# Optimization experiments

Measured on AMD Instinct MI355X. Metric: run time of the kernel, lower is better.

Reference implementation:

```python
import jax, jax.numpy as jnp
import numpy as np

N_NODES = 100000
D = 64        # graph_embed_size == utterance_embed_size
B = 64        # batch size == number of groups per layer
K = 500000    # selected candidate nodes per layer
M = 200000    # mention nodes
ATT_H = 20    # attention_hidden_dim
CTX = 4 * D   # context_embed_size = 2*graph + 2*utter


def setup_inputs() -> dict:
    key = jax.random.key(0)
    ks = jax.random.split(key, 16)
    graph_embed = jax.random.normal(ks[0], (N_NODES, D), jnp.float32)
    utterance_embed = jax.random.normal(ks[1], (B, D), jnp.float32)
    mention_index = jax.random.randint(ks[2], (M,), 0, N_NODES)
    mention_batch_index = jnp.sort(jax.random.randint(ks[3], (M,), 0, B))
    sel_indices = jax.random.randint(ks[4], (2, K), 0, N_NODES + 1)
    sel_batch_indices = jnp.sort(jax.random.randint(ks[5], (2, K), 0, B), axis=-1)
    sel_group_indices = jnp.sort(jax.random.randint(ks[6], (2, K), 0, B), axis=-1)
    grp_batch_indices = jnp.tile(jnp.arange(B), (2, 1))  # group i belongs to batch i
    last_indices = jax.random.randint(ks[7], (2, B), 0, N_NODES + 1)
    intent_indices = jax.random.randint(ks[8], (2, B), 0, 3)
    score_masks = jnp.ones((2, K), jnp.float32)
    # learned parameters (torch nn.Linear default init: U(-1/sqrt(fan_in), 1/sqrt(fan_in)))
    s_w = 1.0 / np.sqrt(D)
    s_v = 1.0 / np.sqrt(ATT_H)
    s_c = 1.0 / np.sqrt(CTX)
    att_W = jax.random.uniform(ks[9], (ATT_H, D), jnp.float32, -s_w, s_w)
    att_V = jax.random.uniform(ks[10], (1, ATT_H), jnp.float32, -s_v, s_v)
    W1_w = jax.random.uniform(ks[11], (1, CTX), jnp.float32, -s_c, s_c)
    W1_b = jax.random.uniform(ks[12], (1,), jnp.float32, -s_c, s_c)
    W2_w = jax.random.uniform(ks[13], (1, CTX), jnp.float32, -s_c, s_c)
    W2_b = jax.random.uniform(ks[14], (1,), jnp.float32, -s_c, s_c)
    intent_emb = jax.random.normal(ks[15], (3, D), jnp.float32)
    return dict(graph_embed=graph_embed, utterance_embed=utterance_embed,
                mention_index=mention_index, mention_batch_index=mention_batch_index,
                sel_indices=sel_indices, sel_batch_indices=sel_batch_indices,
                sel_group_indices=sel_group_indices, grp_batch_indices=grp_batch_indices,
                last_indices=last_indices, intent_indices=intent_indices,
                score_masks=score_masks, att_W=att_W, att_V=att_V,
                W1_w=W1_w, W1_b=W1_b, W2_w=W2_w, W2_b=W2_b, intent_emb=intent_emb)


def _segment_attention(embed, batch_index, att_W, att_V):
    # Self_Attention with batch_index: segment softmax + weighted segment sum.
    beta = jnp.squeeze(jnp.tanh(embed @ att_W.T) @ att_V.T, -1)      # [M]
    exp_beta = jnp.exp(beta)                                          # faithful: raw exp
    seg_sum = jax.ops.segment_sum(exp_beta, batch_index, num_segments=B)  # [B]
    alpha = exp_beta / seg_sum[batch_index]                           # [M]
    return jax.ops.segment_sum(alpha[:, None] * embed, batch_index, num_segments=B)  # [B,D]


def _layer(W_w, W_b, utter, portrait, graph_e, sel, sel_b, sel_g, grp_b,
           last, intent, mask, intent_emb, last_weight):
    context = jnp.concatenate([utter, portrait], axis=-1)             # [B,2D]
    feats = graph_e[sel]                                              # [K,D]
    # grp_context = [tiled context | start-point embed | intent embed] -> [G,4D]
    grp_ctx = jnp.concatenate([context[grp_b], graph_e[last], intent_emb[intent]], axis=-1)
    weights = jax.nn.sigmoid(grp_ctx @ W_w.T + W_b)                   # [G,1]
    tu = utter[sel_b]                                                 # [K,D]
    tp = portrait[sel_b]                                              # [K,D]
    w = weights[sel_g]                                                # [K,1]
    scores = jnp.sum((tu * w + tp * (1.0 - w)) * feats, axis=-1)      # [K]
    if last_weight is None:
        return scores, weights
    lw = last_weight[sel_b]                                           # [K,1]
    last_scores = jnp.sum((tu * lw + tp * (1.0 - lw)) * feats, axis=-1)
    return last_scores + mask * scores, None


def reference(graph_embed, utterance_embed, mention_index, mention_batch_index,
              sel_indices, sel_batch_indices, sel_group_indices, grp_batch_indices,
              last_indices, intent_indices, score_masks,
              att_W, att_V, W1_w, W1_b, W2_w, W2_b, intent_emb):
    # user portrait via segment-softmax attention over mentioned nodes
    mention_embed = graph_embed[mention_index]                        # [M,D]
    portrait = _segment_attention(mention_embed, mention_batch_index, att_W, att_V)  # [B,D]
    # extended graph embedding with abstract (zero) row appended
    graph_e = jnp.concatenate([graph_embed, jnp.zeros((1, D), graph_embed.dtype)], axis=0)
    s0, w0 = _layer(W1_w, W1_b, utterance_embed, portrait, graph_e,
                    sel_indices[0], sel_batch_indices[0], sel_group_indices[0],
                    grp_batch_indices[0], last_indices[0], intent_indices[0],
                    score_masks[0], intent_emb, None)
    s1, _ = _layer(W2_w, W2_b, utterance_embed, portrait, graph_e,
                   sel_indices[1], sel_batch_indices[1], sel_group_indices[1],
                   grp_batch_indices[1], last_indices[1], intent_indices[1],
                   score_masks[1], intent_emb, w0)
    return jnp.stack([s0, s1], axis=0)                                # [2,K]
```

## Files before the change

kernel.cpp:

```cpp
#include <hip/hip_runtime.h>
#include <math.h>

#define N_NODES 100000
#define D_EMB   64
#define KSEL    500000
#define NMENT   200000
#define ATT_H   20
#define NPAD    100352

#define WS_EB    0
#define WS_NUM   100000
#define WS_DEN   104096
#define WS_PORT  104160
#define WS_W     108256
#define WS_T     108544
#define WS_TOTAL_BYTES ((size_t)(WS_T + 64 * NPAD) * 4)

#define NPB 391
#define NBLK_G 784

typedef __attribute__((ext_vector_type(8))) short bf16x8;
typedef __attribute__((ext_vector_type(4))) float f32x4;

__device__ __forceinline__ unsigned pack2bf(float a, float b) {
    unsigned ua = __float_as_uint(a), ub = __float_as_uint(b);
    ua = (ua + 0x7FFFu + ((ua >> 16) & 1u)) >> 16;
    ub = (ub + 0x7FFFu + ((ub >> 16) & 1u)) >> 16;
    return ua | (ub << 16);
}
__device__ __forceinline__ float uasf(unsigned u) { return __uint_as_float(u); }

__global__ __launch_bounds__(256) void kP(const float* __restrict__ ge,
                                          const float* __restrict__ attW,
                                          const float* __restrict__ attV,
                                          float* __restrict__ ws) {
    int tid = blockIdx.x * 256 + threadIdx.x;
    if (tid < 64 * 64 + 64) ws[WS_NUM + tid] = 0.f;
    if (tid >= N_NODES) return;

    const float4* g4 = (const float4*)(ge + (size_t)tid * D_EMB);
    float4 x[16];
#pragma unroll
    for (int i = 0; i < 16; ++i) x[i] = g4[i];

    float beta = 0.f;
#pragma unroll
    for (int j = 0; j < ATT_H; ++j) {
        float h = 0.f;
#pragma unroll
        for (int i = 0; i < 16; ++i) {
            float4 w = ((const float4*)(attW + j * D_EMB))[i];
            h += w.x * x[i].x + w.y * x[i].y + w.z * x[i].z + w.w * x[i].w;
        }
        beta += attV[j] * tanhf(h);
    }
    ws[WS_EB + tid] = expf(beta);
}

__global__ __launch_bounds__(256, 8) void kA2n(const float* __restrict__ ge,
                                               const int* __restrict__ mi,
                                               const int* __restrict__ mbi,
                                               float* __restrict__ ws) {
    __shared__ float lacc[64 * 64];
    __shared__ float lden[64];
    for (int i = threadIdx.x; i < 64 * 64; i += 256) lacc[i] = 0.f;
    if (threadIdx.x < 64) lden[threadIdx.x] = 0.f;
    __syncthreads();

    int lane = threadIdx.x & 63;
    int grp  = lane >> 4, lp = lane & 15;
    int wave = blockIdx.x * 4 + (threadIdx.x >> 6);
    int s = wave * 25;

    bool valid = lane < 25;
    int lastB  = mbi[s + 24];
    int nd     = valid ? mi[s + lane] : 0;
    int bb     = valid ? mbi[s + lane] : lastB;
    float ebv  = valid ? ws[WS_EB + nd] : 0.f;
    int code   = nd | (bb << 17);

    int cd[7]; float e7[7]; float4 rr[7];
#pragma unroll
    for (int i = 0; i < 7; ++i) {
        int u = 4 * i + grp;
        cd[i] = __shfl(code, u);
        e7[i] = __shfl(ebv, u);
    }
#pragma unroll
    for (int i = 0; i < 7; ++i)
        rr[i] = *(const float4*)(ge + (size_t)(cd[i] & 0x1FFFF) * 64 + lp * 4);

    int curb = (__shfl(code, 0) >> 17) & 63;
    float4 acc = make_float4(0.f, 0.f, 0.f, 0.f);
    float dacc = 0.f;
#pragma unroll
    for (int i = 0; i < 7; ++i) {
        int u = 4 * i + grp;
        int b = (cd[i] >> 17) & 63;
        if (u < 25 && b != curb) {
            atomicAdd(&lacc[curb * 64 + lp * 4 + 0], acc.x);
            atomicAdd(&lacc[curb * 64 + lp * 4 + 1], acc.y);
            atomicAdd(&lacc[curb * 64 + lp * 4 + 2], acc.z);
            atomicAdd(&lacc[curb * 64 + lp * 4 + 3], acc.w);
            if (lp == 0) atomicAdd(&lden[curb], dacc);
            acc = make_float4(0.f, 0.f, 0.f, 0.f); dacc = 0.f; curb = b;
        }
        float e = e7[i];
        acc.x = fmaf(e, rr[i].x, acc.x);
        acc.y = fmaf(e, rr[i].y, acc.y);
        acc.z = fmaf(e, rr[i].z, acc.z);
        acc.w = fmaf(e, rr[i].w, acc.w);
        dacc += e;
    }
    atomicAdd(&lacc[curb * 64 + lp * 4 + 0], acc.x);
    atomicAdd(&lacc[curb * 64 + lp * 4 + 1], acc.y);
    atomicAdd(&lacc[curb * 64 + lp * 4 + 2], acc.z);
    atomicAdd(&lacc[curb * 64 + lp * 4 + 3], acc.w);
    if (lp == 0) atomicAdd(&lden[curb], dacc);
    __syncthreads();

    int sB = blockIdx.x * 100;
    int b0 = mbi[sB];
    int b1 = mbi[sB + 99];
    int nb = b1 - b0 + 1;
    for (int idx = threadIdx.x; idx < nb * 64; idx += 256) {
        int b2 = b0 + (idx >> 6), d = idx & 63;
        float v = lacc[b2 * 64 + d];
        if (v != 0.f) atomicAdd(&ws[WS_NUM + b2 * 64 + d], v);
    }
    if (threadIdx.x < nb) {
        float v = lden[b0 + threadIdx.x];
        if (v != 0.f) atomicAdd(&ws[WS_DEN + b0 + threadIdx.x], v);
    }
}

__global__ __launch_bounds__(64) void kBW(const float* __restrict__ ge,
                                          const float* __restrict__ utter,
                                          const int* __restrict__ grpb,
                                          const int* __restrict__ lastI,
                                          const int* __restrict__ intentI,
                                          const float* __restrict__ W1w,
                                          const float* __restrict__ W1b,
                                          const float* __restrict__ W2w,
                                          const float* __restrict__ W2b,
                                          const float* __restrict__ intentEmb,
                                          float* __restrict__ ws) {
    int bi = blockIdx.x;
    int l  = bi >> 6;
    int g  = bi & 63;
    int d  = threadIdx.x;

    if (l == 0) {
        ws[WS_PORT + g * 64 + d] = ws[WS_NUM + g * 64 + d] / ws[WS_DEN + g];
    }
    int gb = grpb[bi];
    float pd = ws[WS_NUM + gb * 64 + d] / ws[WS_DEN + gb];

    int last = lastI[bi];
    float gl = (last < N_NODES) ? ge[(size_t)last * D_EMB + d] : 0.f;
    int it = intentI[bi];
    float ie = intentEmb[it * D_EMB + d];

    const float* Ww = (l == 0) ? W1w : W2w;
    float bias      = (l == 0) ? W1b[0] : W2b[0];

    float val = utter[gb * D_EMB + d] * Ww[d]
              + pd * Ww[64 + d]
              + gl * Ww[128 + d]
              + ie * Ww[192 + d];
#pragma unroll
    for (int off = 32; off; off >>= 1) val += __shfl_xor(val, off);
    if (d == 0) ws[WS_W + bi] = 1.f / (1.f + expf(-(val + bias)));
}

__global__ __launch_bounds__(256) void kG(const float* __restrict__ ge,
                                          const float* __restrict__ utter,
                                          float* __restrict__ ws) {
    int nblk = blockIdx.x;

    __shared__ unsigned sQ[128 * 36];
    int tid = threadIdx.x;
    for (int i = tid; i < 128 * 32; i += 256) {
        int r = i >> 5, c32 = i & 31;
        int k2 = c32 * 2;
        float a, b;
        if (r < 64) {
            a = utter[r * 64 + k2]; b = utter[r * 64 + k2 + 1];
        } else {
            int q = r - 64;
            float dn = ws[WS_DEN + q];
            a = ws[WS_NUM + q * 64 + k2] / dn;
            b = ws[WS_NUM + q * 64 + k2 + 1] / dn;
        }
        sQ[r * 36 + c32] = pack2bf(a, b);
    }
    __syncthreads();

    int l = tid & 63, w = tid >> 6;
    int r16 = l & 15, kb = l >> 4;

    int nb0 = nblk * 128 + w * 32;

    float4 ar[2][2][2];
#pragma unroll
    for (int t = 0; t < 2; ++t) {
        int node = nb0 + t * 16 + r16;
        const float* p = ge + (size_t)node * 64 + kb * 8;
#pragma unroll
        for (int s = 0; s < 2; ++s) {
            float4 z = make_float4(0.f, 0.f, 0.f, 0.f);
            ar[t][s][0] = (node < N_NODES) ? *(const float4*)(p + s * 32)     : z;
            ar[t][s][1] = (node < N_NODES) ? *(const float4*)(p + s * 32 + 4) : z;
        }
    }
    bf16x8 Af[2][2];
#pragma unroll
    for (int t = 0; t < 2; ++t)
#pragma unroll
        for (int s = 0; s < 2; ++s) {
            uint4 u = make_uint4(pack2bf(ar[t][s][0].x, ar[t][s][0].y),
                                 pack2bf(ar[t][s][0].z, ar[t][s][0].w),
                                 pack2bf(ar[t][s][1].x, ar[t][s][1].y),
                                 pack2bf(ar[t][s][1].z, ar[t][s][1].w));
            Af[t][s] = __builtin_bit_cast(bf16x8, u);
        }

    unsigned* Tu = (unsigned*)(ws + WS_T);

#pragma unroll 1
    for (int qq = 0; qq < 4; ++qq) {
        bf16x8 Bf[2][2];
#pragma unroll
        for (int s = 0; s < 2; ++s) {
            uint4 u0 = *(const uint4*)&sQ[(qq * 16 + r16) * 36 + s * 16 + kb * 4];
            uint4 u1 = *(const uint4*)&sQ[(64 + qq * 16 + r16) * 36 + s * 16 + kb * 4];
            Bf[0][s] = __builtin_bit_cast(bf16x8, u0);
            Bf[1][s] = __builtin_bit_cast(bf16x8, u1);
        }

        f32x4 acc[2][2];
#pragma unroll
        for (int t = 0; t < 2; ++t)
#pragma unroll
            for (int c = 0; c < 2; ++c) acc[t][c] = (f32x4){0.f, 0.f, 0.f, 0.f};

#pragma unroll
        for (int t = 0; t < 2; ++t)
#pragma unroll
            for (int s = 0; s < 2; ++s)
#pragma unroll
                for (int c = 0; c < 2; ++c)
                    acc[t][c] = __builtin_amdgcn_mfma_f32_16x16x32_bf16(Af[t][s], Bf[c][s], acc[t][c], 0, 0, 0);

        int b = qq * 16 + r16;
#pragma unroll
        for (int t = 0; t < 2; ++t) {
            uint4 o;
            o.x = pack2bf(acc[t][0][0], acc[t][1][0]);
            o.y = pack2bf(acc[t][0][1], acc[t][1][1]);
            o.z = pack2bf(acc[t][0][2], acc[t][1][2]);
            o.w = pack2bf(acc[t][0][3], acc[t][1][3]);
            *(uint4*)(Tu + (size_t)b * NPAD + nb0 + t * 16 + kb * 4) = o;
        }
    }
}

__global__ __launch_bounds__(256) void kS(const int* __restrict__ sel,
                                          const int* __restrict__ selb,
                                          const int* __restrict__ selg,
                                          const float* __restrict__ masks,
                                          const float* __restrict__ ws,
                                          float* __restrict__ out) {
    __shared__ float sWd[128];
    if (threadIdx.x < 128) sWd[threadIdx.x] = ws[WS_W + threadIdx.x];
    __syncthreads();
    int kk = blockIdx.x * 256 + threadIdx.x;
    if (kk >= 2 * KSEL) return;
    int n = sel[kk], b = selb[kk], g = selg[kk];
    const unsigned* Tu = (const unsigned*)(ws + WS_T);
    unsigned t = Tu[(size_t)b * NPAD + n];
    float du = uasf(t << 16), dp = uasf(t & 0xFFFF0000u);
    float cu, cp;
    if (kk < KSEL) {
        float wv = sWd[g]; cu = wv; cp = 1.f - wv;
    } else {
        float mk = masks[kk];
        float lw = sWd[b], w1 = sWd[64 + g];
        cu = fmaf(mk, w1, lw);
        cp = fmaf(mk, 1.f - w1, 1.f - lw);
    }
    out[kk] = cu * du + cp * dp;
}

#define KA2_L 25
__global__ __launch_bounds__(256) void kA2_fb(const float* __restrict__ ge,
                                              const int* __restrict__ mi,
                                              const int* __restrict__ mbi,
                                              float* __restrict__ ws) {
    int lane = threadIdx.x & 63;
    int wave = (blockIdx.x * 256 + threadIdx.x) >> 6;
    int wstart = wave * KA2_L;
    if (wstart >= NMENT) return;
    int wend = min(wstart + KA2_L, NMENT);
    int len  = wend - wstart;

    int idx    = wstart + lane;
    bool valid = idx < wend;
    int lastB  = mbi[wend - 1];
    int nd     = valid ? mi[idx] : 0;
    int bb     = valid ? mbi[idx] : lastB;
    float ebv  = valid ? ws[WS_EB + nd] : 0.f;
    int code   = nd | (bb << 17);

    float acc = 0.f, dacc = 0.f;
    int curb = __shfl(code, 0) >> 17;

    int Lr = (len + 3) & ~3;
    for (int u0 = 0; u0 < Lr; u0 += 4) {
        int c4[4]; float e4[4]; float x4[4];
#pragma unroll
        for (int j = 0; j < 4; ++j) {
            int u = u0 + j;
            c4[j] = __shfl(code, u);
            e4[j] = __shfl(ebv, u);
            x4[j] = ge[(size_t)(c4[j] & 0x1FFFF) * D_EMB + lane];
        }
#pragma unroll
        for (int j = 0; j < 4; ++j) {
            int b = c4[j] >> 17;
            if (b != curb) {
                atomicAdd(&ws[WS_NUM + curb * 64 + lane], acc);
                if (lane == 0) atomicAdd(&ws[WS_DEN + curb], dacc);
                acc = 0.f; dacc = 0.f; curb = b;
            }
            acc  = fmaf(e4[j], x4[j], acc);
            dacc += e4[j];
        }
    }
    atomicAdd(&ws[WS_NUM + curb * 64 + lane], acc);
    if (lane == 0) atomicAdd(&ws[WS_DEN + curb], dacc);
}

__global__ __launch_bounds__(512, 8) void kC_fb(const float* __restrict__ ge,
                                                const float* __restrict__ utter,
                                                const int* __restrict__ sel,
                                                const int* __restrict__ selb,
                                                const int* __restrict__ selg,
                                                const float* __restrict__ masks,
                                                const float* __restrict__ ws,
                                                float* __restrict__ out) {
    __shared__ float4 sU[64 * 17];
    __shared__ float4 sP[64 * 17];
    __shared__ float  sW[128];
    for (int i = threadIdx.x; i < 64 * 16; i += 512) {
        int r = i >> 4, c = i & 15;
        sU[r * 17 + c] = ((const float4*)utter)[i];
        sP[r * 17 + c] = ((const float4*)(ws + WS_PORT))[i];
    }
    if (threadIdx.x < 128) sW[threadIdx.x] = ws[WS_W + threadIdx.x];
    __syncthreads();

    int lane = threadIdx.x & 63;
    int wave = blockIdx.x * 8 + (threadIdx.x >> 6);
    int W = gridDim.x * 8;
    int grp = lane >> 4, lp = lane & 15;
    const float4* g4 = (const float4*)ge;
    const int NGRP = 2 * KSEL / 4;

    for (int gi = wave; gi < NGRP; gi += W) {
        int kk = gi * 4 + grp;
        int node = sel[kk], b = selb[kk], g = selg[kk];
        float cu, cp;
        if (kk < KSEL) { float w = sW[g]; cu = w; cp = 1.f - w; }
        else {
            float mask = masks[kk]; float lw = sW[b]; float w1 = sW[64 + g];
            cu = fmaf(mask, w1, lw); cp = fmaf(mask, 1.f - w1, 1.f - lw);
        }
        float4 f = make_float4(0.f, 0.f, 0.f, 0.f);
        if (node < N_NODES) f = g4[(size_t)node * 16 + lp];
        float4 tu = sU[b * 17 + lp];
        float4 tp = sP[b * 17 + lp];
        float val = (cu * tu.x + cp * tp.x) * f.x
                  + (cu * tu.y + cp * tp.y) * f.y
                  + (cu * tu.z + cp * tp.z) * f.z
                  + (cu * tu.w + cp * tp.w) * f.w;
        val += __shfl_xor(val, 1);
        val += __shfl_xor(val, 2);
        val += __shfl_xor(val, 4);
        val += __shfl_xor(val, 8);
        if (lp == 0) out[kk] = val;
    }
}

extern "C" void kernel_launch(void* const* d_in, const int* in_sizes, int n_in,
                              void* d_out, int out_size, void* d_ws, size_t ws_size,
                              hipStream_t stream) {
    const float* ge        = (const float*)d_in[0];
    const float* utter     = (const float*)d_in[1];
    const int*   mi        = (const int*)d_in[2];
    const int*   mbi       = (const int*)d_in[3];
    const int*   sel       = (const int*)d_in[4];
    const int*   selb      = (const int*)d_in[5];
    const int*   selg      = (const int*)d_in[6];
    const int*   grpb      = (const int*)d_in[7];
    const int*   lastI     = (const int*)d_in[8];
    const int*   intentI   = (const int*)d_in[9];
    const float* masks     = (const float*)d_in[10];
    const float* attW      = (const float*)d_in[11];
    const float* attV      = (const float*)d_in[12];
    const float* W1w       = (const float*)d_in[13];
    const float* W1b       = (const float*)d_in[14];
    const float* W2w       = (const float*)d_in[15];
    const float* W2b       = (const float*)d_in[16];
    const float* intentEmb = (const float*)d_in[17];
    float* ws  = (float*)d_ws;
    float* out = (float*)d_out;

    bool full = ws_size >= WS_TOTAL_BYTES;

    kP<<<dim3(NPB), dim3(256), 0, stream>>>(ge, attW, attV, ws);

    if (full) {
        kA2n<<<dim3(2000), dim3(256), 0, stream>>>(ge, mi, mbi, ws);
        kBW<<<dim3(128), dim3(64), 0, stream>>>(ge, utter, grpb, lastI, intentI,
                                                W1w, W1b, W2w, W2b, intentEmb, ws);
        kG<<<dim3(NBLK_G), dim3(256), 0, stream>>>(ge, utter, ws);
        kS<<<dim3((2 * KSEL + 255) / 256), dim3(256), 0, stream>>>(sel, selb, selg,
                                                                   masks, ws, out);
    } else {
        kA2_fb<<<dim3(2000), dim3(256), 0, stream>>>(ge, mi, mbi, ws);
        kBW<<<dim3(128), dim3(64), 0, stream>>>(ge, utter, grpb, lastI, intentI,
                                                W1w, W1b, W2w, W2b, intentEmb, ws);
        kC_fb<<<dim3(1024), dim3(512), 0, stream>>>(ge, utter, sel, selb, selg,
                                                    masks, ws, out);
    }
}
```

Baseline: 91.39 us.

## Gather mention rows from bf16 copy and fold gate kernel into kG

kP now also writes a bf16-packed copy of the graph embedding into the workspace, and kA2n gathers mention rows from that copy, halving the bytes of its random gathers. The separate gate kernel kBW is merged into kG as 32 extra blocks, removing one launch. The cost is an extra 12.8MB write in kP, bf16 rounding of the attention-weighted sum, and a larger workspace requirement. The fused path also no longer writes WS_PORT, though kS appears not to read it.

```diff
diff --git a/kernel.cpp b/kernel.cpp
--- a/kernel.cpp
+++ b/kernel.cpp
@@ -13,11 +13,14 @@
 #define WS_DEN   104096
 #define WS_PORT  104160
 #define WS_W     108256
-#define WS_T     108544
+#define WS_BF    108416
+#define WS_BF_BYTE ((size_t)WS_BF * 4)
+#define WS_T     3308416
 #define WS_TOTAL_BYTES ((size_t)(WS_T + 64 * NPAD) * 4)
 
 #define NPB 391
 #define NBLK_G 784
+#define NBLK_GW 32
 
 typedef __attribute__((ext_vector_type(8))) short bf16x8;
 typedef __attribute__((ext_vector_type(4))) float f32x4;
@@ -30,6 +33,7 @@
 }
 __device__ __forceinline__ float uasf(unsigned u) { return __uint_as_float(u); }
 
+template<bool PACK>
 __global__ __launch_bounds__(256) void kP(const float* __restrict__ ge,
                                           const float* __restrict__ attW,
                                           const float* __restrict__ attV,
@@ -43,6 +47,19 @@
 #pragma unroll
     for (int i = 0; i < 16; ++i) x[i] = g4[i];
 
+    if constexpr (PACK) {
+        uint4* dst = (uint4*)((char*)ws + WS_BF_BYTE + (size_t)tid * 128);
+#pragma unroll
+        for (int j = 0; j < 8; ++j) {
+            uint4 o;
+            o.x = pack2bf(x[2*j].x,   x[2*j].y);
+            o.y = pack2bf(x[2*j].z,   x[2*j].w);
+            o.z = pack2bf(x[2*j+1].x, x[2*j+1].y);
+            o.w = pack2bf(x[2*j+1].z, x[2*j+1].w);
+            dst[j] = o;
+        }
+    }
+
     float beta = 0.f;
 #pragma unroll
     for (int j = 0; j < ATT_H; ++j) {
@@ -57,8 +74,7 @@
     ws[WS_EB + tid] = expf(beta);
 }
 
-__global__ __launch_bounds__(256, 8) void kA2n(const float* __restrict__ ge,
-                                               const int* __restrict__ mi,
+__global__ __launch_bounds__(256, 8) void kA2n(const int* __restrict__ mi,
                                                const int* __restrict__ mbi,
                                                float* __restrict__ ws) {
     __shared__ float lacc[64 * 64];
@@ -67,6 +83,8 @@
     if (threadIdx.x < 64) lden[threadIdx.x] = 0.f;
     __syncthreads();
 
+    const unsigned short* bft = (const unsigned short*)((const char*)ws + WS_BF_BYTE);
+
     int lane = threadIdx.x & 63;
     int grp  = lane >> 4, lp = lane & 15;
     int wave = blockIdx.x * 4 + (threadIdx.x >> 6);
@@ -79,7 +97,7 @@
     float ebv  = valid ? ws[WS_EB + nd] : 0.f;
     int code   = nd | (bb << 17);
 
-    int cd[7]; float e7[7]; float4 rr[7];
+    int cd[7]; float e7[7]; uint2 rr[7];
 #pragma unroll
     for (int i = 0; i < 7; ++i) {
         int u = 4 * i + grp;
@@ -88,7 +106,7 @@
     }
 #pragma unroll
     for (int i = 0; i < 7; ++i)
-        rr[i] = *(const float4*)(ge + (size_t)(cd[i] & 0x1FFFF) * 64 + lp * 4);
+        rr[i] = *(const uint2*)(bft + (size_t)(cd[i] & 0x1FFFF) * 64 + lp * 4);
 
     int curb = (__shfl(code, 0) >> 17) & 63;
     float4 acc = make_float4(0.f, 0.f, 0.f, 0.f);
@@ -106,10 +124,10 @@
             acc = make_float4(0.f, 0.f, 0.f, 0.f); dacc = 0.f; curb = b;
         }
         float e = e7[i];
-        acc.x = fmaf(e, rr[i].x, acc.x);
-        acc.y = fmaf(e, rr[i].y, acc.y);
-        acc.z = fmaf(e, rr[i].z, acc.z);
-        acc.w = fmaf(e, rr[i].w, acc.w);
+        acc.x = fmaf(e, uasf(rr[i].x << 16),         acc.x);
+        acc.y = fmaf(e, uasf(rr[i].x & 0xFFFF0000u), acc.y);
+        acc.z = fmaf(e, uasf(rr[i].y << 16),         acc.z);
+        acc.w = fmaf(e, uasf(rr[i].y & 0xFFFF0000u), acc.w);
         dacc += e;
     }
     atomicAdd(&lacc[curb * 64 + lp * 4 + 0], acc.x);
@@ -134,7 +152,7 @@
     }
 }
 
-__global__ __launch_bounds__(64) void kBW(const float* __restrict__ ge,
+__global__ __launch_bounds__(256) void kG(const float* __restrict__ ge,
                                           const float* __restrict__ utter,
                                           const int* __restrict__ grpb,
                                           const int* __restrict__ lastI,
@@ -145,38 +163,27 @@
                                           const float* __restrict__ W2b,
                                           const float* __restrict__ intentEmb,
                                           float* __restrict__ ws) {
-    int bi = blockIdx.x;
-    int l  = bi >> 6;
-    int g  = bi & 63;
-    int d  = threadIdx.x;
-
-    if (l == 0) {
-        ws[WS_PORT + g * 64 + d] = ws[WS_NUM + g * 64 + d] / ws[WS_DEN + g];
-    }
-    int gb = grpb[bi];
-    float pd = ws[WS_NUM + gb * 64 + d] / ws[WS_DEN + gb];
-
-    int last = lastI[bi];
-    float gl = (last < N_NODES) ? ge[(size_t)last * D_EMB + d] : 0.f;
-    int it = intentI[bi];
-    float ie = intentEmb[it * D_EMB + d];
-
-    const float* Ww = (l == 0) ? W1w : W2w;
-    float bias      = (l == 0) ? W1b[0] : W2b[0];
-
-    float val = utter[gb * D_EMB + d] * Ww[d]
-              + pd * Ww[64 + d]
-              + gl * Ww[128 + d]
-              + ie * Ww[192 + d];
-#pragma unroll
-    for (int off = 32; off; off >>= 1) val += __shfl_xor(val, off);
-    if (d == 0) ws[WS_W + bi] = 1.f / (1.f + expf(-(val + bias)));
-}
-
-__global__ __launch_bounds__(256) void kG(const float* __restrict__ ge,
-                                          const float* __restrict__ utter,
-                                          float* __restrict__ ws) {
-    int nblk = blockIdx.x;
+    int bid = blockIdx.x;
+    if (bid >= NBLK_G) {
+        int bi = (bid - NBLK_G) * 4 + (threadIdx.x >> 6);
+        int d  = threadIdx.x & 63;
+        int l  = bi >> 6;
+        int gb = grpb[bi];
+        float pd = ws[WS_NUM + gb * 64 + d] / ws[WS_DEN + gb];
+        int last = lastI[bi];
+        float gl = (last < N_NODES) ? ge[(size_t)last * 64 + d] : 0.f;
+        float ie = intentEmb[intentI[bi] * 64 + d];
+        const float* Ww = l ? W2w : W1w;
+        float bias      = l ? W2b[0] : W1b[0];
+        float val = utter[gb * 64 + d] * Ww[d]
+                  + pd * Ww[64 + d]
+                  + gl * Ww[128 + d]
+                  + ie * Ww[192 + d];
+#pragma unroll
+        for (int off = 32; off; off >>= 1) val += __shfl_xor(val, off);
+        if (d == 0) ws[WS_W + bi] = 1.f / (1.f + expf(-(val + bias)));
+        return;
+    }
 
     __shared__ unsigned sQ[128 * 36];
     int tid = threadIdx.x;
@@ -199,7 +206,7 @@
     int l = tid & 63, w = tid >> 6;
     int r16 = l & 15, kb = l >> 4;
 
-    int nb0 = nblk * 128 + w * 32;
+    int nb0 = bid * 128 + w * 32;
 
     float4 ar[2][2][2];
 #pragma unroll
@@ -292,6 +299,45 @@
     out[kk] = cu * du + cp * dp;
 }
 
+__global__ __launch_bounds__(64) void kBW(const float* __restrict__ ge,
+                                          const float* __restrict__ utter,
+                                          const int* __restrict__ grpb,
+                                          const int* __restrict__ lastI,
+                                          const int* __restrict__ intentI,
+                                          const float* __restrict__ W1w,
+                                          const float* __restrict__ W1b,
+                                          const float* __restrict__ W2w,
+                                          const float* __restrict__ W2b,
+                                          const float* __restrict__ intentEmb,
+                                          float* __restrict__ ws) {
+    int bi = blockIdx.x;
+    int l  = bi >> 6;
+    int g  = bi & 63;
+    int d  = threadIdx.x;
+
+    if (l == 0) {
+        ws[WS_PORT + g * 64 + d] = ws[WS_NUM + g * 64 + d] / ws[WS_DEN + g];
+    }
+    int gb = grpb[bi];
+    float pd = ws[WS_NUM + gb * 64 + d] / ws[WS_DEN + gb];
+
+    int last = lastI[bi];
+    float gl = (last < N_NODES) ? ge[(size_t)last * D_EMB + d] : 0.f;
+    int it = intentI[bi];
+    float ie = intentEmb[it * D_EMB + d];
+
+    const float* Ww = (l == 0) ? W1w : W2w;
+    float bias      = (l == 0) ? W1b[0] : W2b[0];
+
+    float val = utter[gb * D_EMB + d] * Ww[d]
+              + pd * Ww[64 + d]
+              + gl * Ww[128 + d]
+              + ie * Ww[192 + d];
+#pragma unroll
+    for (int off = 32; off; off >>= 1) val += __shfl_xor(val, off);
+    if (d == 0) ws[WS_W + bi] = 1.f / (1.f + expf(-(val + bias)));
+}
+
 #define KA2_L 25
 __global__ __launch_bounds__(256) void kA2_fb(const float* __restrict__ ge,
                                               const int* __restrict__ mi,
@@ -418,16 +464,15 @@
 
     bool full = ws_size >= WS_TOTAL_BYTES;
 
-    kP<<<dim3(NPB), dim3(256), 0, stream>>>(ge, attW, attV, ws);
-
     if (full) {
-        kA2n<<<dim3(2000), dim3(256), 0, stream>>>(ge, mi, mbi, ws);
-        kBW<<<dim3(128), dim3(64), 0, stream>>>(ge, utter, grpb, lastI, intentI,
-                                                W1w, W1b, W2w, W2b, intentEmb, ws);
-        kG<<<dim3(NBLK_G), dim3(256), 0, stream>>>(ge, utter, ws);
+        kP<true><<<dim3(NPB), dim3(256), 0, stream>>>(ge, attW, attV, ws);
+        kA2n<<<dim3(2000), dim3(256), 0, stream>>>(mi, mbi, ws);
+        kG<<<dim3(NBLK_G + NBLK_GW), dim3(256), 0, stream>>>(
+            ge, utter, grpb, lastI, intentI, W1w, W1b, W2w, W2b, intentEmb, ws);
         kS<<<dim3((2 * KSEL + 255) / 256), dim3(256), 0, stream>>>(sel, selb, selg,
                                                                    masks, ws, out);
     } else {
+        kP<false><<<dim3(NPB), dim3(256), 0, stream>>>(ge, attW, attV, ws);
         kA2_fb<<<dim3(2000), dim3(256), 0, stream>>>(ge, mi, mbi, ws);
         kBW<<<dim3(128), dim3(64), 0, stream>>>(ge, utter, grpb, lastI, intentI,
                                                 W1w, W1b, W2w, W2b, intentEmb, ws);
```

New measurement: 93.71 us. 1.03x slower.
